# Kernel tuning notes

Hardware: AMD Instinct MI355X
Metric: run time of the kernel (lower is better)

## Reference

```python
import jax, jax.numpy as jnp
import numpy as np

N, M, D_IN, D_OUT = 8192, 8192, 512, 512


def setup_inputs() -> dict:
    key = jax.random.key(0)
    k1, k2, k3, k4 = jax.random.split(key, 4)
    return {
        "x": jax.random.normal(k1, (N, D_OUT), dtype=jnp.float32),
        "mu": jax.random.normal(k2, (M, D_IN), dtype=jnp.float32),
        "W": jax.random.normal(k3, (D_OUT, D_IN), dtype=jnp.float32),
        "b": jax.random.normal(k4, (D_OUT,), dtype=jnp.float32),
    }


def reference(x, mu, W, b):
    # f_mu: (M, D_out) -- projection + nonlinearity (func = tanh)
    f_mu = jnp.tanh(mu @ W.T + b)
    # measure m[n, m] = -0.5 * ||x_n - f_mu_m||^2, via the matmul expansion
    # (avoids the (N, M, D) diff tensor; same math as sum of squared diffs)
    x_sq = jnp.sum(x * x, axis=-1)            # (N,)
    f_sq = jnp.sum(f_mu * f_mu, axis=-1)      # (M,)
    cross = x @ f_mu.T                        # (N, M)
    m = -0.5 * (x_sq[:, None] - 2.0 * cross + f_sq[None, :])
    # energy: -sum over rows of logsumexp over axis 1
    return -jnp.sum(jax.nn.logsumexp(m, axis=1))
```

## Files before the change

kernel.cpp:

```cpp
#include <hip/hip_runtime.h>

#define D 512
#define NROWS 8192
#define MROWS 8192
#define NCHUNK 8
#define CHUNK_COLS (MROWS / NCHUNK)
#define SWEEPS (CHUNK_COLS / 256)
#define NRB (NROWS / 128)
#define LOG2E 1.4426950408889634f
#define LN2 0.6931471805599453f

typedef float floatx4 __attribute__((ext_vector_type(4)));
typedef __bf16 bf16x8 __attribute__((ext_vector_type(8)));
typedef unsigned uintx4 __attribute__((ext_vector_type(4)));

typedef __attribute__((address_space(1))) void* as1_void_p;
typedef __attribute__((address_space(3))) void* as3_void_p;

__device__ __forceinline__ void async_cp16(const void* g, void* l) {
    __builtin_amdgcn_global_load_lds((as1_void_p)(void*)g, (as3_void_p)l, 16, 0, 0);
}

__device__ __forceinline__ unsigned short f2bf(float f) {
    unsigned u = __float_as_uint(f);
    u += 0x7fffu + ((u >> 16) & 1u);
    return (unsigned short)(u >> 16);
}
__device__ __forceinline__ float bf2f(unsigned short h) {
    return __uint_as_float(((unsigned)h) << 16);
}

__device__ __forceinline__ float fast_tanh(float x) {
    const float xc = fminf(fmaxf(x, -15.0f), 15.0f);
    const float e = __builtin_exp2f(xc * (2.0f * LOG2E));
    return (e - 1.0f) * __builtin_amdgcn_rcpf(e + 1.0f);
}

__device__ __forceinline__ unsigned pack2(float a, float b) {
    return (unsigned)f2bf(a) | ((unsigned)f2bf(b) << 16);
}

#define XBLK (NROWS / 4)
#define MUBLK (MROWS * D / 2048)
#define WBLK (D * D / 2048)
__global__ void k_prep(const float* __restrict__ x,
                       const float* __restrict__ mu,
                       const float* __restrict__ W,
                       unsigned char* __restrict__ xb8,
                       unsigned short* __restrict__ mub,
                       unsigned short* __restrict__ Wb,
                       float* __restrict__ xsq,
                       float* __restrict__ fsq,
                       float* __restrict__ out) {
    const int bid = blockIdx.x;
    const int t = threadIdx.x;
    if (bid < XBLK) {
        if (bid == 0 && t == 0) out[0] = 0.f;
        const int row = bid * 4 + (t >> 6);
        const int lane = t & 63;
        const float4 v0 = ((const float4*)(x + (size_t)row * D))[lane * 2];
        const float4 v1 = ((const float4*)(x + (size_t)row * D))[lane * 2 + 1];
        int p0 = 0, p1 = 0;
        p0 = __builtin_amdgcn_cvt_pk_fp8_f32(v0.x * LOG2E, v0.y * LOG2E, p0, false);
        p0 = __builtin_amdgcn_cvt_pk_fp8_f32(v0.z * LOG2E, v0.w * LOG2E, p0, true);
        p1 = __builtin_amdgcn_cvt_pk_fp8_f32(v1.x * LOG2E, v1.y * LOG2E, p1, false);
        p1 = __builtin_amdgcn_cvt_pk_fp8_f32(v1.z * LOG2E, v1.w * LOG2E, p1, true);
        uint2 o; o.x = (unsigned)p0; o.y = (unsigned)p1;
        ((uint2*)(xb8 + (size_t)row * D))[lane] = o;
        float q, s = 0.f;
        q = __builtin_amdgcn_cvt_f32_fp8(p0, 0); s += q * q;
        q = __builtin_amdgcn_cvt_f32_fp8(p0, 1); s += q * q;
        q = __builtin_amdgcn_cvt_f32_fp8(p0, 2); s += q * q;
        q = __builtin_amdgcn_cvt_f32_fp8(p0, 3); s += q * q;
        q = __builtin_amdgcn_cvt_f32_fp8(p1, 0); s += q * q;
        q = __builtin_amdgcn_cvt_f32_fp8(p1, 1); s += q * q;
        q = __builtin_amdgcn_cvt_f32_fp8(p1, 2); s += q * q;
        q = __builtin_amdgcn_cvt_f32_fp8(p1, 3); s += q * q;
        #pragma unroll
        for (int m = 1; m < 64; m <<= 1) s += __shfl_xor(s, m);
        if (lane == 0) xsq[row] = s;
    } else if (bid < XBLK + MUBLK) {
        const size_t i = ((size_t)(bid - XBLK) * 256 + t) * 2;
        const float4 v0 = ((const float4*)mu)[i];
        const float4 v1 = ((const float4*)mu)[i + 1];
        uintx4 o;
        o.x = pack2(v0.x, v0.y); o.y = pack2(v0.z, v0.w);
        o.z = pack2(v1.x, v1.y); o.w = pack2(v1.z, v1.w);
        ((uintx4*)mub)[i / 2] = o;
    } else {
        const int wb = bid - XBLK - MUBLK;
        const size_t i = ((size_t)wb * 256 + t) * 2;
        const float4 v0 = ((const float4*)W)[i];
        const float4 v1 = ((const float4*)W)[i + 1];
        uintx4 o;
        o.x = pack2(v0.x, v0.y); o.y = pack2(v0.z, v0.w);
        o.z = pack2(v1.x, v1.y); o.w = pack2(v1.z, v1.w);
        ((uintx4*)Wb)[i / 2] = o;
        if (t < 64) fsq[wb * 64 + t] = 0.f;
    }
}

__global__ __launch_bounds__(256, 2)
void k_fgemm(const unsigned short* __restrict__ mub,
             const unsigned short* __restrict__ Wb,
             const float* __restrict__ bias,
             unsigned char* __restrict__ fb8,
             float* __restrict__ fsq) {
    __shared__ unsigned short Ab[128 * 32];
    __shared__ unsigned short Bb[64 * 32];

    const int tid = threadIdx.x;
    const int wave = tid >> 6;
    const int lane = tid & 63;
    const int wr = wave >> 1, wc = wave & 1;
    const int g = lane >> 4;
    const int lm = lane & 15;

    const int row0 = blockIdx.x * 128;
    const int col0 = blockIdx.y * 64;

    const int srow = tid >> 2;
    const int gsrc = (tid & 3) ^ ((srow >> 1) & 3);
    const unsigned short* gA = mub + (size_t)(row0 + srow) * D + gsrc * 8;
    const unsigned short* gB = Wb  + (size_t)(col0 + srow) * D + gsrc * 8;
    char* lA = ((char*)Ab) + wave * 1024;
    char* lB = ((char*)Bb) + wave * 1024;

    const int xsel = (lm >> 1) & 3;
    const unsigned short* fragA = Ab + (64 * wr + lm) * 32 + (g ^ xsel) * 8;
    const unsigned short* fragB = Bb + (32 * wc + lm) * 32 + (g ^ xsel) * 8;

    floatx4 acc[4][2];
    const floatx4 zz = {0.f, 0.f, 0.f, 0.f};
    #pragma unroll
    for (int i = 0; i < 4; ++i)
        #pragma unroll
        for (int j = 0; j < 2; ++j) acc[i][j] = zz;

    for (int kt = 0; kt < 16; ++kt) {
        const int k0 = kt * 32;
        async_cp16(gA + k0, lA);
        async_cp16(gA + 64 * D + k0, lA + 4096);
        async_cp16(gB + k0, lB);
        __syncthreads();
        bf16x8 af[4], bfr[2];
        #pragma unroll
        for (int i = 0; i < 4; ++i) af[i] = *(const bf16x8*)(fragA + i * 512);
        #pragma unroll
        for (int j = 0; j < 2; ++j) bfr[j] = *(const bf16x8*)(fragB + j * 512);
        #pragma unroll
        for (int i = 0; i < 4; ++i)
            #pragma unroll
            for (int j = 0; j < 2; ++j)
                acc[i][j] = __builtin_amdgcn_mfma_f32_16x16x32_bf16(af[i], bfr[j], acc[i][j], 0, 0, 0);
        __syncthreads();
    }

    float bcol[2];
    #pragma unroll
    for (int j = 0; j < 2; ++j) bcol[j] = bias[col0 + 32 * wc + 16 * j + lm];
    #pragma unroll
    for (int i = 0; i < 4; ++i) {
        #pragma unroll
        for (int r = 0; r < 4; ++r) {
            const int row = row0 + 64 * wr + 16 * i + 4 * g + r;
            float sq = 0.f;
            #pragma unroll
            for (int j = 0; j < 2; ++j) {
                const int col = col0 + 32 * wc + 16 * j + lm;
                const float tv = fast_tanh(acc[i][j][r] + bcol[j]);
                const int pk = __builtin_amdgcn_cvt_pk_fp8_f32(tv, tv, 0, false);
                fb8[(size_t)row * D + col] = (unsigned char)(pk & 0xff);
                const float qf = __builtin_amdgcn_cvt_f32_fp8(pk, 0);
                sq += qf * qf;
            }
            #pragma unroll
            for (int d = 1; d < 16; d <<= 1) sq += __shfl_xor(sq, d);
            if (lm == 0) atomicAdd(fsq + row, sq);
        }
    }
}

__global__ __launch_bounds__(256, 2)
void k_cross(const unsigned char* __restrict__ xb8,
             const unsigned char* __restrict__ fb8,
             const float* __restrict__ fsq,
             float* __restrict__ pmax,
             float* __restrict__ psum) {
    __shared__ char Ab[128 * 64];
    __shared__ char Bb[256 * 64];
    __shared__ float mbuf[128], sbuf[128];

    const int tid = threadIdx.x;
    const int wave = tid >> 6;
    const int lane = tid & 63;
    const int wr = wave >> 1, wc = wave & 1;
    const int g = lane >> 4;
    const int lm = lane & 15;

    const int row0 = blockIdx.x * 128;
    const int chunk = blockIdx.y;

    const int srow = tid >> 2;
    const int gsrc = ((tid & 3) ^ ((srow >> 1) & 3)) * 16;
    const unsigned char* gA = xb8 + (size_t)(row0 + srow) * D + gsrc;
    char* lA = Ab + wave * 1024;
    char* lB = Bb + wave * 1024;

    const int xsel = (lm >> 1) & 3;
    const char* fragA = Ab + (64 * wr + lm) * 64;
    const char* fragB = Bb + (128 * wc + lm) * 64;
    const int sub = (g & 1) * 8;

    float m_loc[4][4], s_loc[4][4];
    #pragma unroll
    for (int i = 0; i < 4; ++i)
        #pragma unroll
        for (int r = 0; r < 4; ++r) { m_loc[i][r] = -__builtin_inff(); s_loc[i][r] = 0.f; }

    for (int st = 0; st < SWEEPS; ++st) {
        const int col0 = chunk * CHUNK_COLS + st * 256;
        const unsigned char* gB = fb8 + (size_t)(col0 + srow) * D + gsrc;

        floatx4 acc[4][8];
        const floatx4 zz = {0.f, 0.f, 0.f, 0.f};
        #pragma unroll
        for (int i = 0; i < 4; ++i)
            #pragma unroll
            for (int j = 0; j < 8; ++j) acc[i][j] = zz;

        for (int kt = 0; kt < 8; ++kt) {
            const int k0 = kt * 64;
            async_cp16(gA + k0, lA);
            async_cp16(gA + (size_t)64 * D + k0, lA + 4096);
            #pragma unroll
            for (int h4 = 0; h4 < 4; ++h4)
                async_cp16(gB + (size_t)(64 * h4) * D + k0, lB + 4096 * h4);
            __syncthreads();
            #pragma unroll
            for (int h = 0; h < 2; ++h) {
                const int pg = ((h * 2 + (g >> 1)) ^ xsel) * 16 + sub;
                long a0 = *(const long*)(fragA + 0 * 1024 + pg);
                long a1 = *(const long*)(fragA + 1 * 1024 + pg);
                long a2 = *(const long*)(fragA + 2 * 1024 + pg);
                long a3 = *(const long*)(fragA + 3 * 1024 + pg);
                #pragma unroll
                for (int j = 0; j < 8; ++j) {
                    const long bj = *(const long*)(fragB + j * 1024 + pg);
                    acc[0][j] = __builtin_amdgcn_mfma_f32_16x16x32_fp8_fp8(a0, bj, acc[0][j], 0, 0, 0);
                    acc[1][j] = __builtin_amdgcn_mfma_f32_16x16x32_fp8_fp8(a1, bj, acc[1][j], 0, 0, 0);
                    acc[2][j] = __builtin_amdgcn_mfma_f32_16x16x32_fp8_fp8(a2, bj, acc[2][j], 0, 0, 0);
                    acc[3][j] = __builtin_amdgcn_mfma_f32_16x16x32_fp8_fp8(a3, bj, acc[3][j], 0, 0, 0);
                }
            }
            __syncthreads();
        }

        float hf[8];
        #pragma unroll
        for (int j = 0; j < 8; ++j)
            hf[j] = 0.5f * LOG2E * fsq[col0 + 128 * wc + 16 * j + lm];
        #pragma unroll
        for (int i = 0; i < 4; ++i) {
            #pragma unroll
            for (int r = 0; r < 4; ++r) {
                float v[8];
                float mm = -__builtin_inff();
                #pragma unroll
                for (int j = 0; j < 8; ++j) {
                    v[j] = acc[i][j][r] - hf[j];
                    mm = fmaxf(mm, v[j]);
                }
                const float nm = fmaxf(m_loc[i][r], mm);
                float s = s_loc[i][r] * __builtin_exp2f(m_loc[i][r] - nm);
                #pragma unroll
                for (int j = 0; j < 8; ++j) s += __builtin_exp2f(v[j] - nm);
                s_loc[i][r] = s;
                m_loc[i][r] = nm;
            }
        }
    }

    #pragma unroll
    for (int i = 0; i < 4; ++i) {
        #pragma unroll
        for (int r = 0; r < 4; ++r) {
            float m = m_loc[i][r], s = s_loc[i][r];
            #pragma unroll
            for (int d = 1; d < 16; d <<= 1) {
                const float om = __shfl_xor(m, d);
                const float os = __shfl_xor(s, d);
                const float nm = fmaxf(m, om);
                s = s * __builtin_exp2f(m - nm) + os * __builtin_exp2f(om - nm);
                m = nm;
            }
            m_loc[i][r] = m; s_loc[i][r] = s;
        }
    }
    if (wc == 0 && lm == 0) {
        #pragma unroll
        for (int i = 0; i < 4; ++i)
            #pragma unroll
            for (int r = 0; r < 4; ++r) {
                const int rl = 64 * wr + 16 * i + 4 * g + r;
                mbuf[rl] = m_loc[i][r]; sbuf[rl] = s_loc[i][r];
            }
    }
    __syncthreads();
    if (wc == 1 && lm == 0) {
        #pragma unroll
        for (int i = 0; i < 4; ++i)
            #pragma unroll
            for (int r = 0; r < 4; ++r) {
                const int rl = 64 * wr + 16 * i + 4 * g + r;
                const float om = mbuf[rl], os = sbuf[rl];
                float m = m_loc[i][r], s = s_loc[i][r];
                const float nm = fmaxf(m, om);
                s = s * __builtin_exp2f(m - nm) + os * __builtin_exp2f(om - nm);
                pmax[(size_t)(row0 + rl) * NCHUNK + chunk] = nm;
                psum[(size_t)(row0 + rl) * NCHUNK + chunk] = s;
            }
    }
}

__global__ void k_finish(const float* __restrict__ pmax,
                         const float* __restrict__ psum,
                         const float* __restrict__ xsq,
                         float* __restrict__ out) {
    const int row = blockIdx.x * 256 + threadIdx.x;
    const float4* pm4 = (const float4*)(pmax + (size_t)row * NCHUNK);
    const float4* ps4 = (const float4*)(psum + (size_t)row * NCHUNK);
    float pm[NCHUNK], ps[NCHUNK];
    #pragma unroll
    for (int c = 0; c < NCHUNK / 4; ++c) {
        const float4 a = pm4[c], b = ps4[c];
        pm[4*c] = a.x; pm[4*c+1] = a.y; pm[4*c+2] = a.z; pm[4*c+3] = a.w;
        ps[4*c] = b.x; ps[4*c+1] = b.y; ps[4*c+2] = b.z; ps[4*c+3] = b.w;
    }
    float gm = -__builtin_inff();
    #pragma unroll
    for (int c = 0; c < NCHUNK; ++c) gm = fmaxf(gm, pm[c]);
    float s = 0.f;
    #pragma unroll
    for (int c = 0; c < NCHUNK; ++c) s += ps[c] * __builtin_exp2f(pm[c] - gm);
    float lse = LN2 * (gm + __builtin_log2f(s)) - 0.5f * (LN2 * LN2) * xsq[row];
    #pragma unroll
    for (int m = 1; m < 64; m <<= 1) lse += __shfl_xor(lse, m);
    __shared__ float ws4[4];
    if ((threadIdx.x & 63) == 0) ws4[threadIdx.x >> 6] = lse;
    __syncthreads();
    if (threadIdx.x == 0) atomicAdd(out, -(ws4[0] + ws4[1] + ws4[2] + ws4[3]));
}

extern "C" void kernel_launch(void* const* d_in, const int* in_sizes, int n_in,
                              void* d_out, int out_size, void* d_ws, size_t ws_size,
                              hipStream_t stream) {
    const float* x  = (const float*)d_in[0];
    const float* mu = (const float*)d_in[1];
    const float* W  = (const float*)d_in[2];
    const float* b  = (const float*)d_in[3];

    char* ws = (char*)d_ws;
    unsigned char*  xb8 = (unsigned char*)(ws);
    unsigned char*  fb8 = (unsigned char*)(ws + (4u << 20));
    unsigned short* mub = (unsigned short*)(ws + (8u << 20));
    unsigned short* Wb  = (unsigned short*)(ws + (16u << 20));
    float* xsq  = (float*)(ws + (17u << 20));
    float* fsq  = xsq + NROWS;
    float* pmax = fsq + MROWS;
    float* psum = pmax + (size_t)NROWS * NCHUNK;

    float* out = (float*)d_out;

    hipLaunchKernelGGL(k_prep, dim3(XBLK + MUBLK + WBLK), dim3(256), 0, stream,
                       x, mu, W, xb8, mub, Wb, xsq, fsq, out);
    hipLaunchKernelGGL(k_fgemm, dim3(MROWS / 128, D / 64), dim3(256), 0, stream,
                       mub, Wb, b, fb8, fsq);
    hipLaunchKernelGGL(k_cross, dim3(NRB, NCHUNK), dim3(256), 0, stream,
                       xb8, fb8, fsq, pmax, psum);
    hipLaunchKernelGGL(k_finish, dim3(NROWS / 256), dim3(256), 0, stream,
                       pmax, psum, xsq, out);
}
```

Before: 168.4 us.

## Use 16x16x128 scaled FP8 MFMA in cross GEMM and overlap x prep with fgemm

The cross kernel now stages 128-wide K tiles in shared memory, with a new 8-way XOR swizzle. It issues the MI355 scaled f8f6f4 16x16x128 MFMA with unit scales instead of the 16x16x32 fp8 MFMA, which cuts the instruction count and the number of barriers per K loop. The x-to-FP8 conversion moves out of the first prep kernel into the f-projection GEMM launch as extra blocks, so it runs concurrently with the GEMM. The cost is doubled shared memory in k_cross (about 48KB), which may lower occupancy.

```diff
diff --git a/kernel.cpp b/kernel.cpp
--- a/kernel.cpp
+++ b/kernel.cpp
@@ -13,6 +13,7 @@
 typedef float floatx4 __attribute__((ext_vector_type(4)));
 typedef __bf16 bf16x8 __attribute__((ext_vector_type(8)));
 typedef unsigned uintx4 __attribute__((ext_vector_type(4)));
+typedef int intx8 __attribute__((ext_vector_type(8)));
 
 typedef __attribute__((address_space(1))) void* as1_void_p;
 typedef __attribute__((address_space(3))) void* as3_void_p;
@@ -40,24 +41,55 @@
     return (unsigned)f2bf(a) | ((unsigned)f2bf(b) << 16);
 }
 
-#define XBLK (NROWS / 4)
 #define MUBLK (MROWS * D / 2048)
 #define WBLK (D * D / 2048)
-__global__ void k_prep(const float* __restrict__ x,
-                       const float* __restrict__ mu,
-                       const float* __restrict__ W,
-                       unsigned char* __restrict__ xb8,
-                       unsigned short* __restrict__ mub,
-                       unsigned short* __restrict__ Wb,
-                       float* __restrict__ xsq,
-                       float* __restrict__ fsq,
-                       float* __restrict__ out) {
+__global__ void k_convmw(const float* __restrict__ mu,
+                         const float* __restrict__ W,
+                         unsigned short* __restrict__ mub,
+                         unsigned short* __restrict__ Wb,
+                         float* __restrict__ fsq,
+                         float* __restrict__ out) {
     const int bid = blockIdx.x;
     const int t = threadIdx.x;
-    if (bid < XBLK) {
-        if (bid == 0 && t == 0) out[0] = 0.f;
-        const int row = bid * 4 + (t >> 6);
-        const int lane = t & 63;
+    if (bid < MUBLK) {
+        const size_t i = ((size_t)bid * 256 + t) * 2;
+        const float4 v0 = ((const float4*)mu)[i];
+        const float4 v1 = ((const float4*)mu)[i + 1];
+        uintx4 o;
+        o.x = pack2(v0.x, v0.y); o.y = pack2(v0.z, v0.w);
+        o.z = pack2(v1.x, v1.y); o.w = pack2(v1.z, v1.w);
+        ((uintx4*)mub)[i / 2] = o;
+    } else {
+        const int wb = bid - MUBLK;
+        if (wb == 0 && t == 0) out[0] = 0.f;
+        const size_t i = ((size_t)wb * 256 + t) * 2;
+        const float4 v0 = ((const float4*)W)[i];
+        const float4 v1 = ((const float4*)W)[i + 1];
+        uintx4 o;
+        o.x = pack2(v0.x, v0.y); o.y = pack2(v0.z, v0.w);
+        o.z = pack2(v1.x, v1.y); o.w = pack2(v1.z, v1.w);
+        ((uintx4*)Wb)[i / 2] = o;
+        if (t < 64) fsq[wb * 64 + t] = 0.f;
+    }
+}
+
+#define FGB 512
+#define XBLK (NROWS / 4)
+__global__ __launch_bounds__(256, 2)
+void k_fgemm_xprep(const unsigned short* __restrict__ mub,
+                   const unsigned short* __restrict__ Wb,
+                   const float* __restrict__ bias,
+                   const float* __restrict__ x,
+                   unsigned char* __restrict__ fb8,
+                   unsigned char* __restrict__ xb8,
+                   float* __restrict__ fsq,
+                   float* __restrict__ xsq) {
+    const int bid = blockIdx.x;
+    const int tid = threadIdx.x;
+
+    if (bid >= FGB) {
+        const int row = (bid - FGB) * 4 + (tid >> 6);
+        const int lane = tid & 63;
         const float4 v0 = ((const float4*)(x + (size_t)row * D))[lane * 2];
         const float4 v1 = ((const float4*)(x + (size_t)row * D))[lane * 2 + 1];
         int p0 = 0, p1 = 0;
@@ -79,45 +111,20 @@
         #pragma unroll
         for (int m = 1; m < 64; m <<= 1) s += __shfl_xor(s, m);
         if (lane == 0) xsq[row] = s;
-    } else if (bid < XBLK + MUBLK) {
-        const size_t i = ((size_t)(bid - XBLK) * 256 + t) * 2;
-        const float4 v0 = ((const float4*)mu)[i];
-        const float4 v1 = ((const float4*)mu)[i + 1];
-        uintx4 o;
-        o.x = pack2(v0.x, v0.y); o.y = pack2(v0.z, v0.w);
-        o.z = pack2(v1.x, v1.y); o.w = pack2(v1.z, v1.w);
-        ((uintx4*)mub)[i / 2] = o;
-    } else {
-        const int wb = bid - XBLK - MUBLK;
-        const size_t i = ((size_t)wb * 256 + t) * 2;
-        const float4 v0 = ((const float4*)W)[i];
-        const float4 v1 = ((const float4*)W)[i + 1];
-        uintx4 o;
-        o.x = pack2(v0.x, v0.y); o.y = pack2(v0.z, v0.w);
-        o.z = pack2(v1.x, v1.y); o.w = pack2(v1.z, v1.w);
-        ((uintx4*)Wb)[i / 2] = o;
-        if (t < 64) fsq[wb * 64 + t] = 0.f;
-    }
-}
-
-__global__ __launch_bounds__(256, 2)
-void k_fgemm(const unsigned short* __restrict__ mub,
-             const unsigned short* __restrict__ Wb,
-             const float* __restrict__ bias,
-             unsigned char* __restrict__ fb8,
-             float* __restrict__ fsq) {
+        return;
+    }
+
     __shared__ unsigned short Ab[128 * 32];
     __shared__ unsigned short Bb[64 * 32];
 
-    const int tid = threadIdx.x;
     const int wave = tid >> 6;
     const int lane = tid & 63;
     const int wr = wave >> 1, wc = wave & 1;
     const int g = lane >> 4;
     const int lm = lane & 15;
 
-    const int row0 = blockIdx.x * 128;
-    const int col0 = blockIdx.y * 64;
+    const int row0 = (bid & 63) * 128;
+    const int col0 = (bid >> 6) * 64;
 
     const int srow = tid >> 2;
     const int gsrc = (tid & 3) ^ ((srow >> 1) & 3);
@@ -187,8 +194,8 @@
              const float* __restrict__ fsq,
              float* __restrict__ pmax,
              float* __restrict__ psum) {
-    __shared__ char Ab[128 * 64];
-    __shared__ char Bb[256 * 64];
+    __shared__ char Ab[128 * 128];
+    __shared__ char Bb[256 * 128];
     __shared__ float mbuf[128], sbuf[128];
 
     const int tid = threadIdx.x;
@@ -201,16 +208,29 @@
     const int row0 = blockIdx.x * 128;
     const int chunk = blockIdx.y;
 
-    const int srow = tid >> 2;
-    const int gsrc = ((tid & 3) ^ ((srow >> 1) & 3)) * 16;
-    const unsigned char* gA = xb8 + (size_t)(row0 + srow) * D + gsrc;
-    char* lA = Ab + wave * 1024;
-    char* lB = Bb + wave * 1024;
-
-    const int xsel = (lm >> 1) & 3;
-    const char* fragA = Ab + (64 * wr + lm) * 64;
-    const char* fragB = Bb + (128 * wc + lm) * 64;
-    const int sub = (g & 1) * 8;
+    const unsigned char* pA[4];
+    char* dA[4];
+    size_t offB[8];
+    char* dB[8];
+    #pragma unroll
+    for (int p = 0; p < 4; ++p) {
+        const int row = 32 * wave + 8 * p + (lane >> 3);
+        const int srcg = (lane & 7) ^ ((row >> 1) & 7);
+        pA[p] = xb8 + (size_t)(row0 + row) * D + srcg * 16;
+        dA[p] = Ab + wave * 4096 + p * 1024 + lane * 16;
+    }
+    #pragma unroll
+    for (int p = 0; p < 8; ++p) {
+        const int row = 64 * wave + 8 * p + (lane >> 3);
+        const int srcg = (lane & 7) ^ ((row >> 1) & 7);
+        offB[p] = (size_t)row * D + srcg * 16;
+        dB[p] = Bb + wave * 8192 + p * 1024 + lane * 16;
+    }
+
+    const int f8 = (lm >> 1) & 7;
+    const int pg0 = ((2 * g) ^ f8) * 16;
+    const char* fragA = Ab + (64 * wr + lm) * 128;
+    const char* fragB = Bb + (128 * wc + lm) * 128;
 
     float m_loc[4][4], s_loc[4][4];
     #pragma unroll
@@ -220,7 +240,7 @@
 
     for (int st = 0; st < SWEEPS; ++st) {
         const int col0 = chunk * CHUNK_COLS + st * 256;
-        const unsigned char* gB = fb8 + (size_t)(col0 + srow) * D + gsrc;
+        const unsigned char* gBbase = fb8 + (size_t)col0 * D;
 
         floatx4 acc[4][8];
         const floatx4 zz = {0.f, 0.f, 0.f, 0.f};
@@ -229,29 +249,36 @@
             #pragma unroll
             for (int j = 0; j < 8; ++j) acc[i][j] = zz;
 
-        for (int kt = 0; kt < 8; ++kt) {
-            const int k0 = kt * 64;
-            async_cp16(gA + k0, lA);
-            async_cp16(gA + (size_t)64 * D + k0, lA + 4096);
-            #pragma unroll
-            for (int h4 = 0; h4 < 4; ++h4)
-                async_cp16(gB + (size_t)(64 * h4) * D + k0, lB + 4096 * h4);
+        for (int kt = 0; kt < 4; ++kt) {
+            const int k0 = kt * 128;
+            #pragma unroll
+            for (int p = 0; p < 4; ++p) async_cp16(pA[p] + k0, dA[p]);
+            #pragma unroll
+            for (int p = 0; p < 8; ++p) async_cp16(gBbase + offB[p] + k0, dB[p]);
             __syncthreads();
-            #pragma unroll
-            for (int h = 0; h < 2; ++h) {
-                const int pg = ((h * 2 + (g >> 1)) ^ xsel) * 16 + sub;
-                long a0 = *(const long*)(fragA + 0 * 1024 + pg);
-                long a1 = *(const long*)(fragA + 1 * 1024 + pg);
-                long a2 = *(const long*)(fragA + 2 * 1024 + pg);
-                long a3 = *(const long*)(fragA + 3 * 1024 + pg);
-                #pragma unroll
-                for (int j = 0; j < 8; ++j) {
-                    const long bj = *(const long*)(fragB + j * 1024 + pg);
-                    acc[0][j] = __builtin_amdgcn_mfma_f32_16x16x32_fp8_fp8(a0, bj, acc[0][j], 0, 0, 0);
-                    acc[1][j] = __builtin_amdgcn_mfma_f32_16x16x32_fp8_fp8(a1, bj, acc[1][j], 0, 0, 0);
-                    acc[2][j] = __builtin_amdgcn_mfma_f32_16x16x32_fp8_fp8(a2, bj, acc[2][j], 0, 0, 0);
-                    acc[3][j] = __builtin_amdgcn_mfma_f32_16x16x32_fp8_fp8(a3, bj, acc[3][j], 0, 0, 0);
-                }
+
+            intx8 av[4];
+            #pragma unroll
+            for (int i = 0; i < 4; ++i) {
+                const char* pa = fragA + i * 2048;
+                const int4 lo = *(const int4*)(pa + pg0);
+                const int4 hi = *(const int4*)(pa + (pg0 ^ 16));
+                av[i] = (intx8){lo.x, lo.y, lo.z, lo.w, hi.x, hi.y, hi.z, hi.w};
+            }
+            #pragma unroll
+            for (int j = 0; j < 8; ++j) {
+                const char* pb = fragB + j * 2048;
+                const int4 lo = *(const int4*)(pb + pg0);
+                const int4 hi = *(const int4*)(pb + (pg0 ^ 16));
+                const intx8 bv = {lo.x, lo.y, lo.z, lo.w, hi.x, hi.y, hi.z, hi.w};
+                acc[0][j] = __builtin_amdgcn_mfma_scale_f32_16x16x128_f8f6f4(
+                    av[0], bv, acc[0][j], 0, 0, 0, 0x7f7f7f7f, 0, 0x7f7f7f7f);
+                acc[1][j] = __builtin_amdgcn_mfma_scale_f32_16x16x128_f8f6f4(
+                    av[1], bv, acc[1][j], 0, 0, 0, 0x7f7f7f7f, 0, 0x7f7f7f7f);
+                acc[2][j] = __builtin_amdgcn_mfma_scale_f32_16x16x128_f8f6f4(
+                    av[2], bv, acc[2][j], 0, 0, 0, 0x7f7f7f7f, 0, 0x7f7f7f7f);
+                acc[3][j] = __builtin_amdgcn_mfma_scale_f32_16x16x128_f8f6f4(
+                    av[3], bv, acc[3][j], 0, 0, 0, 0x7f7f7f7f, 0, 0x7f7f7f7f);
             }
             __syncthreads();
         }
@@ -372,10 +399,10 @@
 
     float* out = (float*)d_out;
 
-    hipLaunchKernelGGL(k_prep, dim3(XBLK + MUBLK + WBLK), dim3(256), 0, stream,
-                       x, mu, W, xb8, mub, Wb, xsq, fsq, out);
-    hipLaunchKernelGGL(k_fgemm, dim3(MROWS / 128, D / 64), dim3(256), 0, stream,
-                       mub, Wb, b, fb8, fsq);
+    hipLaunchKernelGGL(k_convmw, dim3(MUBLK + WBLK), dim3(256), 0, stream,
+                       mu, W, mub, Wb, fsq, out);
+    hipLaunchKernelGGL(k_fgemm_xprep, dim3(FGB + XBLK), dim3(256), 0, stream,
+                       mub, Wb, b, x, fb8, xb8, fsq, xsq);
     hipLaunchKernelGGL(k_cross, dim3(NRB, NCHUNK), dim3(256), 0, stream,
                        xb8, fb8, fsq, pmax, psum);
     hipLaunchKernelGGL(k_finish, dim3(NROWS / 256), dim3(256), 0, stream,
```

After: 150.6 us. 10.6% less time.
